# Performance work log

Measured on AMD Instinct MI355X. Metric: run time of the kernel, lower is better.

Reference implementation:

```python
import jax, jax.numpy as jnp
import numpy as np

EPS = 1e-08


def setup_inputs() -> dict:
    key = jax.random.key(0)
    k1, k2, k3 = jax.random.split(key, 3)
    B_img, B_txt, D = 8192, 8192, 512
    img_feature = jax.random.normal(k1, (B_img, D), dtype=jnp.float32)
    text_feature = jax.random.normal(k2, (B_txt, D), dtype=jnp.float32)
    text_lens = jax.random.randint(k3, (B_txt,), 1, 40, dtype=jnp.int32)
    return {"img_feature": img_feature, "text_feature": text_feature, "text_lens": text_lens}


def reference(img_feature, text_feature, text_lens):
    # Pairwise cosine similarity: equivalent to the original expand+mul+sum,
    # expressed as a GEMM of the raw features followed by norm division.
    # w12[i,j] = <img_i, txt_j>; sim = w12 / max(|img_i|*|txt_j|, eps)
    w12 = jnp.einsum('id,jd->ij', img_feature, text_feature)  # [B_img, B_txt]
    w1 = jnp.linalg.norm(img_feature, axis=-1)                # [B_img]
    w2 = jnp.linalg.norm(text_feature, axis=-1)               # [B_txt]
    denom = jnp.maximum(w1[:, None] * w2[None, :], EPS)
    return w12 / denom
```

## Files before the change

kernel.cpp:

```cpp
#include <hip/hip_runtime.h>
#include <hip/hip_bf16.h>

#define M 8192
#define N 8192
#define K 512
#define BM 256
#define BN 256
#define BK 64
#define NT (K / BK)
#define EPSV 1e-8f

typedef __attribute__((ext_vector_type(8))) short bf16x8;
typedef __attribute__((ext_vector_type(4))) float f32x4;
typedef __attribute__((ext_vector_type(8))) unsigned short us8;

__device__ inline void gload_lds16(const void* g, void* l) {
  __builtin_amdgcn_global_load_lds(
      (const __attribute__((address_space(1))) unsigned int*)g,
      (__attribute__((address_space(3))) unsigned int*)l, 16, 0, 0);
}

#define BARRIER()                          \
  do {                                     \
    asm volatile("" ::: "memory");         \
    __builtin_amdgcn_s_barrier();          \
    asm volatile("" ::: "memory");         \
  } while (0)

__global__ __launch_bounds__(256) void prep_kernel(const float* __restrict__ in,
                                                   unsigned short* __restrict__ outb,
                                                   float* __restrict__ norms) {
  const int gw = (blockIdx.x * 256 + threadIdx.x) >> 6;
  const int lane = threadIdx.x & 63;
  const float4* rp4 = (const float4*)(in + (size_t)gw * K);
  float4 v0 = rp4[lane * 2];
  float4 v1 = rp4[lane * 2 + 1];
  float ss = v0.x * v0.x + v0.y * v0.y + v0.z * v0.z + v0.w * v0.w +
             v1.x * v1.x + v1.y * v1.y + v1.z * v1.z + v1.w * v1.w;
  float f[8] = {v0.x, v0.y, v0.z, v0.w, v1.x, v1.y, v1.z, v1.w};
  us8 o;
#pragma unroll
  for (int i = 0; i < 8; ++i) {
    __hip_bfloat16 b = __float2bfloat16(f[i]);
    o[i] = *(unsigned short*)&b;
  }
  *(us8*)(outb + (size_t)gw * K + lane * 8) = o;
#pragma unroll
  for (int off = 32; off > 0; off >>= 1) ss += __shfl_down(ss, off, 64);
  if (lane == 0) norms[gw] = sqrtf(ss);
}

__global__ __launch_bounds__(512, 2) void gemm_kernel(const unsigned short* __restrict__ A,
                                                      const unsigned short* __restrict__ B,
                                                      const float* __restrict__ w1,
                                                      const float* __restrict__ w2,
                                                      float* __restrict__ C) {
  __shared__ __align__(128) unsigned short As[2][2][128 * 64];
  __shared__ __align__(128) unsigned short Bs[2][2][128 * 64];

  const int tid = threadIdx.x;
  const int wave = tid >> 6;
  const int lane = tid & 63;
  const int wr = wave >> 2;
  const int wc = wave & 3;
  const int fr = lane & 15;
  const int fq = lane >> 4;

  const int bid = blockIdx.x;
  const int swz = (bid & 7) * ((M / BM) * (N / BN) / 8) + (bid >> 3);
  const int bRow = (swz / (N / BN)) * BM;
  const int bCol = (swz % (N / BN)) * BN;

  const int r0 = tid >> 3;
  const int r1 = 64 + (tid >> 3);
  const int csw = ((tid & 7) * 16) ^ ((r0 & 7) << 4);

  auto stageA = [&](int buf, int half, int kt) {
    gload_lds16(A + (size_t)(bRow + half * 128 + r0) * K + kt * BK + (csw >> 1),
                (char*)&As[buf][half][0] + wave * 1024);
    gload_lds16(A + (size_t)(bRow + half * 128 + r1) * K + kt * BK + (csw >> 1),
                (char*)&As[buf][half][0] + 8192 + wave * 1024);
  };
  auto stageB = [&](int buf, int half, int kt) {
    gload_lds16(B + (size_t)(bCol + half * 128 + r0) * K + kt * BK + (csw >> 1),
                (char*)&Bs[buf][half][0] + wave * 1024);
    gload_lds16(B + (size_t)(bCol + half * 128 + r1) * K + kt * BK + (csw >> 1),
                (char*)&Bs[buf][half][0] + 8192 + wave * 1024);
  };
  auto ldA = [&](int buf, int r, int cb) -> bf16x8 {
    return *(const bf16x8*)((const char*)&As[buf][wr][0] + r * 128 + (cb ^ ((r & 7) << 4)));
  };
  auto ldB = [&](int buf, int r, int cb) -> bf16x8 {
    return *(const bf16x8*)((const char*)&Bs[buf][wc >> 1][0] + r * 128 + (cb ^ ((r & 7) << 4)));
  };

  f32x4 acc[8][4] = {};
  bf16x8 a[4][2], bLo[2][2], bHi[2][2];
  const int bRowB = (wc & 1) * 64;

  stageA(0, 0, 0);
  stageA(0, 1, 0);
  stageB(0, 0, 0);
  stageB(0, 1, 0);
  stageB(1, 0, 1);
  stageB(1, 1, 1);
  asm volatile("s_waitcnt vmcnt(4)" ::: "memory");
  BARRIER();

#define MFMA_Q(MB, BARR, NB)                                                      \
  _Pragma("unroll") for (int kk = 0; kk < 2; ++kk)                                \
      _Pragma("unroll") for (int m = 0; m < 4; ++m)                               \
          _Pragma("unroll") for (int n = 0; n < 2; ++n)                           \
              acc[(MB) + m][(NB) + n] = __builtin_amdgcn_mfma_f32_16x16x32_bf16(  \
                  a[m][kk], BARR[n][kk], acc[(MB) + m][(NB) + n], 0, 0, 0);

#pragma unroll
  for (int t = 0; t < NT; ++t) {
    const int cur = t & 1, nxt = cur ^ 1;

#pragma unroll
    for (int m = 0; m < 4; ++m)
#pragma unroll
      for (int kk = 0; kk < 2; ++kk) a[m][kk] = ldA(cur, m * 16 + fr, kk * 64 + fq * 16);
#pragma unroll
    for (int n = 0; n < 2; ++n)
#pragma unroll
      for (int kk = 0; kk < 2; ++kk)
        bLo[n][kk] = ldB(cur, bRowB + n * 16 + fr, kk * 64 + fq * 16);
    if (t + 1 < NT) stageA(nxt, 0, t + 1);
    BARRIER();
    __builtin_amdgcn_s_setprio(1);
    MFMA_Q(0, bLo, 0)
    __builtin_amdgcn_s_setprio(0);
    BARRIER();

#pragma unroll
    for (int n = 0; n < 2; ++n)
#pragma unroll
      for (int kk = 0; kk < 2; ++kk)
        bHi[n][kk] = ldB(cur, bRowB + 32 + n * 16 + fr, kk * 64 + fq * 16);
    if (t + 1 < NT) stageA(nxt, 1, t + 1);
    BARRIER();
    __builtin_amdgcn_s_setprio(1);
    MFMA_Q(0, bHi, 2)
    __builtin_amdgcn_s_setprio(0);
    BARRIER();

#pragma unroll
    for (int m = 0; m < 4; ++m)
#pragma unroll
      for (int kk = 0; kk < 2; ++kk) a[m][kk] = ldA(cur, 64 + m * 16 + fr, kk * 64 + fq * 16);
    if (t + 2 < NT) stageB(cur, 0, t + 2);
    BARRIER();
    __builtin_amdgcn_s_setprio(1);
    MFMA_Q(4, bLo, 0)
    __builtin_amdgcn_s_setprio(0);
    BARRIER();

    if (t + 2 < NT) stageB(cur, 1, t + 2);
    BARRIER();
    __builtin_amdgcn_s_setprio(1);
    MFMA_Q(4, bHi, 2)
    __builtin_amdgcn_s_setprio(0);
    if (t < NT - 2) {
      asm volatile("s_waitcnt vmcnt(4)" ::: "memory");
    } else if (t == NT - 2) {
      asm volatile("s_waitcnt vmcnt(0)" ::: "memory");
    }
    BARRIER();
  }
#undef MFMA_Q

#pragma unroll
  for (int m = 0; m < 8; ++m) {
    const int row0 = bRow + wr * 128 + m * 16 + fq * 4;
    float w1v[4];
#pragma unroll
    for (int r = 0; r < 4; ++r) w1v[r] = w1[row0 + r];
#pragma unroll
    for (int n = 0; n < 4; ++n) {
      const int col = bCol + wc * 64 + n * 16 + fr;
      const float w2v = w2[col];
      f32x4 v = acc[m][n];
#pragma unroll
      for (int r = 0; r < 4; ++r)
        C[(size_t)(row0 + r) * N + col] = v[r] / fmaxf(w1v[r] * w2v, EPSV);
    }
  }
}

extern "C" void kernel_launch(void* const* d_in, const int* in_sizes, int n_in,
                              void* d_out, int out_size, void* d_ws, size_t ws_size,
                              hipStream_t stream) {
  (void)in_sizes; (void)n_in; (void)out_size; (void)ws_size;
  const float* img = (const float*)d_in[0];
  const float* txt = (const float*)d_in[1];
  float* out = (float*)d_out;

  unsigned short* Abf = (unsigned short*)d_ws;
  unsigned short* Bbf = Abf + (size_t)M * K;
  float* w1 = (float*)(Bbf + (size_t)N * K);
  float* w2 = w1 + M;

  prep_kernel<<<M / 4, 256, 0, stream>>>(img, Abf, w1);
  prep_kernel<<<N / 4, 256, 0, stream>>>(txt, Bbf, w2);
  gemm_kernel<<<(M / BM) * (N / BN), 512, 0, stream>>>(Abf, Bbf, w1, w2, out);
}
```

Measured before the change: 125.4 us.

## Merge prep launches, remap GEMM tiles per XCD, use nontemporal output stores

The two prep launches become one kernel that chooses the image or text half from the block index, removing one launch and its gap. The GEMM tile mapping changes so each XCD owns a band of four output columns (1024 columns of B) and walks down the rows, aiming for B reuse in that XCD's L2. The 256MB fp32 output is written with nontemporal stores to avoid polluting the cache. The new tile order may reduce A reuse compared with the previous swizzle.

```diff
diff --git a/kernel.cpp b/kernel.cpp
--- a/kernel.cpp
+++ b/kernel.cpp
@@ -27,10 +27,19 @@
     asm volatile("" ::: "memory");         \
   } while (0)
 
-__global__ __launch_bounds__(256) void prep_kernel(const float* __restrict__ in,
-                                                   unsigned short* __restrict__ outb,
-                                                   float* __restrict__ norms) {
-  const int gw = (blockIdx.x * 256 + threadIdx.x) >> 6;
+__global__ __launch_bounds__(256) void prep_kernel(const float* __restrict__ img,
+                                                   const float* __restrict__ txt,
+                                                   unsigned short* __restrict__ Abf,
+                                                   unsigned short* __restrict__ Bbf,
+                                                   float* __restrict__ w1,
+                                                   float* __restrict__ w2) {
+  const int half = blockIdx.x >> 11;
+  const int lb = blockIdx.x & 2047;
+  const float* in = half ? txt : img;
+  unsigned short* outb = half ? Bbf : Abf;
+  float* norms = half ? w2 : w1;
+
+  const int gw = (lb * 256 + threadIdx.x) >> 6;
   const int lane = threadIdx.x & 63;
   const float4* rp4 = (const float4*)(in + (size_t)gw * K);
   float4 v0 = rp4[lane * 2];
@@ -66,10 +75,10 @@
   const int fr = lane & 15;
   const int fq = lane >> 4;
 
-  const int bid = blockIdx.x;
-  const int swz = (bid & 7) * ((M / BM) * (N / BN) / 8) + (bid >> 3);
-  const int bRow = (swz / (N / BN)) * BM;
-  const int bCol = (swz % (N / BN)) * BN;
+  const int xcd = blockIdx.x & 7;
+  const int idx = blockIdx.x >> 3;
+  const int bRow = (idx >> 2) * BM;
+  const int bCol = (xcd * 4 + (idx & 3)) * BN;
 
   const int r0 = tid >> 3;
   const int r1 = 64 + (tid >> 3);
@@ -184,7 +193,8 @@
       f32x4 v = acc[m][n];
 #pragma unroll
       for (int r = 0; r < 4; ++r)
-        C[(size_t)(row0 + r) * N + col] = v[r] / fmaxf(w1v[r] * w2v, EPSV);
+        __builtin_nontemporal_store(v[r] / fmaxf(w1v[r] * w2v, EPSV),
+                                    &C[(size_t)(row0 + r) * N + col]);
     }
   }
 }
@@ -202,7 +212,6 @@
   float* w1 = (float*)(Bbf + (size_t)N * K);
   float* w2 = w1 + M;
 
-  prep_kernel<<<M / 4, 256, 0, stream>>>(img, Abf, w1);
-  prep_kernel<<<N / 4, 256, 0, stream>>>(txt, Bbf, w2);
+  prep_kernel<<<4096, 256, 0, stream>>>(img, txt, Abf, Bbf, w1, w2);
   gemm_kernel<<<(M / BM) * (N / BN), 512, 0, stream>>>(Abf, Bbf, w1, w2, out);
 }
```

Result: slower. 149.6 us (+19.3%).
